# Kernel tuning notes

Hardware: AMD Instinct MI355X
Metric: run time of the kernel (lower is better)

The kernel has to match this reference:

```python
import jax, jax.numpy as jnp
import numpy as np

B, H, W, C = 32, 32, 32, 512
N_GROUPS = 32
EPS = 1e-5


def group_norm(x, scale, bias, n_groups=N_GROUPS, eps=EPS):
    b, h, w, c = x.shape
    xg = x.reshape(b, h, w, n_groups, c // n_groups)
    mean = xg.mean(axis=(1, 2, 4), keepdims=True)
    var = xg.var(axis=(1, 2, 4), keepdims=True)
    xg = (xg - mean) * jax.lax.rsqrt(var + eps)
    return xg.reshape(b, h, w, c) * scale + bias


def setup_inputs() -> dict:
    key = jax.random.key(0)
    ks = jax.random.split(key, 8)
    x = jax.random.normal(ks[0], (B, H, W, C), dtype=jnp.float32)
    t = jax.random.normal(ks[1], (B,), dtype=jnp.float32)
    gn_scale = jnp.ones((C,), jnp.float32)
    gn_bias = jnp.zeros((C,), jnp.float32)
    w_qkv = jax.random.normal(ks[2], (C, 3 * C), dtype=jnp.float32) / np.sqrt(C)
    b_qkv = jnp.zeros((3 * C,), jnp.float32)
    w_out = jax.random.normal(ks[3], (C, C), dtype=jnp.float32) / np.sqrt(C)
    b_out = jnp.zeros((C,), jnp.float32)
    return {"x": x, "t": t, "gn_scale": gn_scale, "gn_bias": gn_bias,
            "w_qkv": w_qkv, "b_qkv": b_qkv, "w_out": w_out, "b_out": b_out}


def reference(x, t, gn_scale, gn_bias, w_qkv, b_qkv, w_out, b_out):
    b, h, w, c = x.shape
    z = group_norm(x, gn_scale, gn_bias)
    qkv = jnp.einsum('bhwc,cd->bhwd', z, w_qkv) + b_qkv  # [b,h,w,3C]
    q, k, v = jnp.split(qkv, 3, axis=-1)
    # single-head spatial attention over all h*w positions
    attn = jnp.einsum('bhwc,bHWc->bhwHW', q, k) / jnp.sqrt(jnp.asarray(c, x.dtype))
    attn = jax.nn.softmax(attn.reshape(b, h, w, h * w), axis=-1)
    attn = attn.reshape(b, h, w, h, w)
    scores = jnp.einsum('bhwHW,bHWc->bhwc', attn, v)
    scores = jnp.einsum('bhwc,cd->bhwd', scores, w_out) + b_out
    return x + scores
```

## Files before the change

### kernel.cpp

```cpp
#include <hip/hip_runtime.h>

typedef unsigned short u16;
typedef short bf16x8 __attribute__((ext_vector_type(8)));
typedef float f32x4 __attribute__((ext_vector_type(4)));

__device__ __forceinline__ u16 f2bf(float f) {
  union { float f; unsigned u; } c; c.f = f;
  unsigned r = (c.u + 0x7FFFu + ((c.u >> 16) & 1u)) >> 16;
  return (u16)r;
}
__device__ __forceinline__ float bf2f(u16 h) {
  union { unsigned u; float f; } c; c.u = ((unsigned)h) << 16;
  return c.f;
}
__device__ __forceinline__ void gload16(const void* g, void* l) {
  __builtin_amdgcn_global_load_lds(
      (const __attribute__((address_space(1))) unsigned*)g,
      (__attribute__((address_space(3))) unsigned*)l, 16, 0, 0);
}

__global__ __launch_bounds__(256) void prep_weights(
    const float* __restrict__ w_qkv, const float* __restrict__ w_out,
    u16* __restrict__ wqkvT, u16* __restrict__ woutT) {
  int i = blockIdx.x * 256 + threadIdx.x;
  const int T1 = 1536 * 512;
  if (i < T1) {
    int n = i >> 9, c = i & 511;
    wqkvT[i] = f2bf(w_qkv[(size_t)c * 1536 + n]);
  } else {
    int j = i - T1;
    int n = j >> 9, c = j & 511;
    woutT[j] = f2bf(w_out[(size_t)c * 512 + n]);
  }
}

__global__ __launch_bounds__(256) void groupnorm_k(
    const float* __restrict__ x, const float* __restrict__ scale,
    const float* __restrict__ bias, u16* __restrict__ z) {
  const int blk = blockIdx.x, b = blk >> 5, g = blk & 31;
  const float* xb = x + (size_t)b * 524288 + g * 16;
  u16* zb = z + (size_t)b * 524288 + g * 16;
  const int tid = threadIdx.x, lane = tid & 63, wid = tid >> 6;

  float4 vv[16];
  float s = 0.f, ss = 0.f;
#pragma unroll
  for (int i = 0; i < 16; ++i) {
    int e = (i * 256 + tid) * 4;
    int hw = e >> 4, j = e & 15;
    vv[i] = *(const float4*)&xb[(size_t)hw * 512 + j];
    s += vv[i].x + vv[i].y + vv[i].z + vv[i].w;
    ss += vv[i].x * vv[i].x + vv[i].y * vv[i].y + vv[i].z * vv[i].z + vv[i].w * vv[i].w;
  }
#pragma unroll
  for (int off = 32; off; off >>= 1) {
    s += __shfl_xor(s, off);
    ss += __shfl_xor(ss, off);
  }
  __shared__ float rs[4], rq[4];
  if (!lane) { rs[wid] = s; rq[wid] = ss; }
  __syncthreads();
  float S_ = rs[0] + rs[1] + rs[2] + rs[3];
  float Q_ = rq[0] + rq[1] + rq[2] + rq[3];
  const float inv_n = 1.f / 16384.f;
  float mean = S_ * inv_n;
  float var = Q_ * inv_n - mean * mean;
  float rstd = rsqrtf(var + 1e-5f);

  int j0 = (tid * 4) & 15;
  float sc0 = scale[g * 16 + j0 + 0] * rstd, sc1 = scale[g * 16 + j0 + 1] * rstd;
  float sc2 = scale[g * 16 + j0 + 2] * rstd, sc3 = scale[g * 16 + j0 + 3] * rstd;
  float bi0 = bias[g * 16 + j0 + 0] - mean * sc0, bi1 = bias[g * 16 + j0 + 1] - mean * sc1;
  float bi2 = bias[g * 16 + j0 + 2] - mean * sc2, bi3 = bias[g * 16 + j0 + 3] - mean * sc3;
#pragma unroll
  for (int i = 0; i < 16; ++i) {
    int e = (i * 256 + tid) * 4;
    int hw = e >> 4, j = e & 15;
    ushort4 o;
    o.x = f2bf(vv[i].x * sc0 + bi0);
    o.y = f2bf(vv[i].y * sc1 + bi1);
    o.z = f2bf(vv[i].z * sc2 + bi2);
    o.w = f2bf(vv[i].w * sc3 + bi3);
    *(ushort4*)&zb[(size_t)hw * 512 + j] = o;
  }
}

#define QSCALE 0.04419417382415922f

template <int EPI>
__global__ __launch_bounds__(512, 2) void gemm8p(
    const u16* __restrict__ A, const u16* __restrict__ Bt,
    int gx, int gxy, int N, int K,
    long long sAb, long long sBb, long long sCb,
    const float* __restrict__ bias, const float* __restrict__ resid,
    u16* __restrict__ qb, u16* __restrict__ kb, u16* __restrict__ vt,
    u16* __restrict__ outb, float* __restrict__ outf) {
  int nb = gridDim.x, orig = blockIdx.x, id = orig;
  if (!(nb & 7)) { int chunk = nb >> 3; id = (orig & 7) * chunk + (orig >> 3); }
  int z = id / gxy; int r2 = id - z * gxy;
  int by = r2 / gx; int bx = r2 - by * gx;

  const u16* Ab = A + (size_t)z * sAb;
  const u16* Bb = Bt + (size_t)z * sBb;

  __shared__ u16 As[2][2][8192];
  __shared__ u16 Bs[2][2][8192];

  const int tid = threadIdx.x;
  const int lane = tid & 63, wid = tid >> 6;
  const int wm = wid & 1, wn = wid >> 1;
  const int l15 = lane & 15, l4 = lane >> 4;
  const int m0 = by * 256, n0 = bx * 256;

  const int own_is_b = wid >> 2;
  const int own_h = (wid >> 1) & 1;
  const int prow = ((wid & 1) << 6) | lane;
  const int srow = prow >> 3;
  const int scol = ((prow & 7) ^ (srow & 7)) << 3;
  const u16* own_base = (own_is_b ? Bb : Ab) +
      (size_t)((own_is_b ? n0 : m0) + own_h * 128 + srow) * K + scol;
  const int ldsbase = ((wid & 1) << 6) * 8;

  f32x4 acc[8][4];
#pragma unroll
  for (int i = 0; i < 8; ++i)
#pragma unroll
    for (int j = 0; j < 4; ++j)
#pragma unroll
      for (int r = 0; r < 4; ++r) acc[i][j][r] = 0.f;

  const int NT = K >> 6;

  auto stage = [&](int k0, int buf) {
    u16* l0 = (own_is_b ? &Bs[buf][own_h][0] : &As[buf][own_h][0]) + ldsbase;
    const u16* g0 = own_base + k0;
#pragma unroll
    for (int j = 0; j < 8; ++j)
      gload16(g0 + (size_t)(j * 16) * K, l0 + j * 1024);
  };

  stage(0, 0);
  asm volatile("s_waitcnt vmcnt(0)" ::: "memory");
  __builtin_amdgcn_s_barrier();

  for (int t = 0; t < NT; ++t) {
    const int cur = t & 1;
    const bool pre = (t + 1 < NT);
    const u16* Ah = &As[cur][wm][0];
    const u16* Bh = &Bs[cur][wn >> 1][0];
    const int rbB = (wn & 1) << 6;
    bf16x8 bq[4][2];
#pragma unroll
    for (int q = 0; q < 4; ++q) {
      bf16x8 af[2][2];
      if (q == 0) {
#pragma unroll
        for (int i = 0; i < 4; ++i) {
          const int rr = rbB + i * 16 + l15;
          const int sw = rr & 7;
          bq[i][0] = *(const bf16x8*)&Bh[rr * 64 + ((l4 ^ sw) << 3)];
          bq[i][1] = *(const bf16x8*)&Bh[rr * 64 + (((4 + l4) ^ sw) << 3)];
        }
      }
#pragma unroll
      for (int j = 0; j < 2; ++j) {
        const int rr = (q * 2 + j) * 16 + l15;
        const int sw = rr & 7;
        af[j][0] = *(const bf16x8*)&Ah[rr * 64 + ((l4 ^ sw) << 3)];
        af[j][1] = *(const bf16x8*)&Ah[rr * 64 + (((4 + l4) ^ sw) << 3)];
      }
      if (q == 0 && pre) stage((t + 1) << 6, cur ^ 1);
      __builtin_amdgcn_s_barrier();
      asm volatile("s_waitcnt lgkmcnt(0)" ::: "memory");
      __builtin_amdgcn_sched_barrier(0);
      __builtin_amdgcn_s_setprio(1);
#pragma unroll
      for (int j = 0; j < 2; ++j)
#pragma unroll
        for (int ni = 0; ni < 4; ++ni) {
          acc[q * 2 + j][ni] = __builtin_amdgcn_mfma_f32_16x16x32_bf16(
              af[j][0], bq[ni][0], acc[q * 2 + j][ni], 0, 0, 0);
          acc[q * 2 + j][ni] = __builtin_amdgcn_mfma_f32_16x16x32_bf16(
              af[j][1], bq[ni][1], acc[q * 2 + j][ni], 0, 0, 0);
        }
      __builtin_amdgcn_s_setprio(0);
      if (q == 3 && pre) asm volatile("s_waitcnt vmcnt(0)" ::: "memory");
      __builtin_amdgcn_s_barrier();
    }
  }

#pragma unroll
  for (int mi = 0; mi < 8; ++mi) {
#pragma unroll
    for (int ni = 0; ni < 4; ++ni) {
      const int gr0 = m0 + wm * 128 + mi * 16 + l4 * 4;
      const int gc = n0 + wn * 64 + ni * 16 + l15;
      if (EPI == 0) {
        const int bsel = gc >> 9, cin = gc & 511;
        const float bs = bias[gc];
        if (bsel < 2) {
          u16* dst = bsel ? kb : qb;
#pragma unroll
          for (int r = 0; r < 4; ++r) {
            float vvv = acc[mi][ni][r] + bs;
            if (bsel == 0) vvv *= QSCALE;
            dst[(size_t)(gr0 + r) * 512 + cin] = f2bf(vvv);
          }
        } else {
          ushort4 o;
          o.x = f2bf(acc[mi][ni][0] + bs);
          o.y = f2bf(acc[mi][ni][1] + bs);
          o.z = f2bf(acc[mi][ni][2] + bs);
          o.w = f2bf(acc[mi][ni][3] + bs);
          const int bb = gr0 >> 10, p = gr0 & 1023;
          *(ushort4*)&vt[(size_t)bb * 524288 + (size_t)cin * 1024 + p] = o;
        }
      } else if (EPI == 1) {
#pragma unroll
        for (int r = 0; r < 4; ++r)
          outb[(size_t)z * sCb + (size_t)(gr0 + r) * N + gc] = f2bf(acc[mi][ni][r]);
      } else {
#pragma unroll
        for (int r = 0; r < 4; ++r)
          outf[(size_t)(gr0 + r) * N + gc] =
              acc[mi][ni][r] + bias[gc] + resid[(size_t)(gr0 + r) * N + gc];
      }
    }
  }
}

__global__ __launch_bounds__(256) void softmax_rows(u16* __restrict__ S) {
  const size_t row = blockIdx.x;
  u16* p = S + row * 1024;
  const int tid = threadIdx.x, lane = tid & 63, wid = tid >> 6;
  ushort4 raw = ((const ushort4*)p)[tid];
  float v0 = bf2f(raw.x), v1 = bf2f(raw.y), v2 = bf2f(raw.z), v3 = bf2f(raw.w);
  float mx = fmaxf(fmaxf(v0, v1), fmaxf(v2, v3));
#pragma unroll
  for (int off = 32; off; off >>= 1) mx = fmaxf(mx, __shfl_xor(mx, off));
  __shared__ float red[8];
  if (!lane) red[wid] = mx;
  __syncthreads();
  mx = fmaxf(fmaxf(red[0], red[1]), fmaxf(red[2], red[3]));
  float e0 = __expf(v0 - mx), e1 = __expf(v1 - mx), e2 = __expf(v2 - mx), e3 = __expf(v3 - mx);
  float s = e0 + e1 + e2 + e3;
#pragma unroll
  for (int off = 32; off; off >>= 1) s += __shfl_xor(s, off);
  if (!lane) red[4 + wid] = s;
  __syncthreads();
  float inv = 1.0f / (red[4] + red[5] + red[6] + red[7]);
  ushort4 o;
  o.x = f2bf(e0 * inv); o.y = f2bf(e1 * inv); o.z = f2bf(e2 * inv); o.w = f2bf(e3 * inv);
  ((ushort4*)p)[tid] = o;
}

extern "C" void kernel_launch(void* const* d_in, const int* in_sizes, int n_in,
                              void* d_out, int out_size, void* d_ws, size_t ws_size,
                              hipStream_t stream) {
  const float* x = (const float*)d_in[0];
  const float* gn_scale = (const float*)d_in[2];
  const float* gn_bias = (const float*)d_in[3];
  const float* w_qkv = (const float*)d_in[4];
  const float* b_qkv = (const float*)d_in[5];
  const float* w_out = (const float*)d_in[6];
  const float* b_out = (const float*)d_in[7];
  float* out = (float*)d_out;

  char* ws = (char*)d_ws;
  const size_t MB = 1024ull * 1024ull;
  u16* qb = (u16*)(ws + 0 * MB);
  u16* kb = (u16*)(ws + 32 * MB);
  u16* vt = (u16*)(ws + 64 * MB);
  u16* zO = (u16*)(ws + 128 * MB);
  u16* S = (u16*)(ws + 160 * MB);
  u16* wqkvT = (u16*)(ws + 224 * MB);
  u16* woutT = (u16*)(ws + 226 * MB);

  prep_weights<<<4096, 256, 0, stream>>>(w_qkv, w_out, wqkvT, woutT);
  groupnorm_k<<<1024, 256, 0, stream>>>(x, gn_scale, gn_bias, zO);

  gemm8p<0><<<768, 512, 0, stream>>>(
      zO, wqkvT, 6, 768, 1536, 512, 0, 0, 0, b_qkv, nullptr,
      qb, kb, vt, nullptr, nullptr);

  gemm8p<1><<<512, 512, 0, stream>>>(
      qb, kb, 4, 16, 1024, 512, 1024 * 512, 1024 * 512, 1024 * 1024,
      nullptr, nullptr, nullptr, nullptr, nullptr, S, nullptr);

  softmax_rows<<<32768, 256, 0, stream>>>(S);

  gemm8p<1><<<256, 512, 0, stream>>>(
      S, vt, 2, 8, 512, 1024, 1024 * 1024, 512 * 1024, 1024 * 512,
      nullptr, nullptr, nullptr, nullptr, nullptr, zO, nullptr);

  gemm8p<2><<<256, 512, 0, stream>>>(
      zO, woutT, 2, 256, 512, 512, 0, 0, 0, b_out, x,
      nullptr, nullptr, nullptr, nullptr, out);
}
```

Baseline: 269.5 us.

## Spread GEMM tile loads across all waves and interleave per-quarter prefetch

Instead of having each wave own one half-tile and issue all prefetch loads at the first sub-step, every thread now loads a slice of each of the four half-tiles. The loads are spread over the four MFMA quarters, and the B tiles are prefetched two iterations ahead, using partial vmcnt waits. This spreads memory traffic more evenly across the K loop and keeps more loads in flight. The scheduling barrier is also removed. In exchange, the vmcnt bookkeeping is fragile, and B prefetch two steps ahead writes into the same double buffer, which risks a hazard if the ordering is wrong.

Result: slower. 278.8 us (+3.5%).

```diff
diff --git a/kernel.cpp b/kernel.cpp
--- a/kernel.cpp
+++ b/kernel.cpp
@@ -111,15 +111,21 @@
   const int wm = wid & 1, wn = wid >> 1;
   const int l15 = lane & 15, l4 = lane >> 4;
   const int m0 = by * 256, n0 = bx * 256;
-
-  const int own_is_b = wid >> 2;
-  const int own_h = (wid >> 1) & 1;
-  const int prow = ((wid & 1) << 6) | lane;
-  const int srow = prow >> 3;
-  const int scol = ((prow & 7) ^ (srow & 7)) << 3;
-  const u16* own_base = (own_is_b ? Bb : Ab) +
-      (size_t)((own_is_b ? n0 : m0) + own_h * 128 + srow) * K + scol;
-  const int ldsbase = ((wid & 1) << 6) * 8;
+  const int NT = K >> 6;
+
+  const int srow = tid >> 3;
+  const int scol = ((tid & 7) ^ (srow & 7)) << 3;
+
+  auto stageH = [&](int tt, int h) {
+    if (tt >= NT) return;
+    const int bsel = tt & 1;
+    u16* lds = (h >= 2 ? &Bs[bsel][h - 2][0] : &As[bsel][h][0]) + tid * 8;
+    const u16* gb = (h >= 2 ? Bb : Ab);
+    const int rb = (h >= 2 ? n0 + (h - 2) * 128 : m0 + h * 128) + srow;
+    const int k0 = (tt << 6) + scol;
+    gload16(gb + (size_t)rb * K + k0, lds);
+    gload16(gb + (size_t)(rb + 64) * K + k0, lds + 512 * 8);
+  };
 
   f32x4 acc[8][4];
 #pragma unroll
@@ -129,23 +135,13 @@
 #pragma unroll
       for (int r = 0; r < 4; ++r) acc[i][j][r] = 0.f;
 
-  const int NT = K >> 6;
-
-  auto stage = [&](int k0, int buf) {
-    u16* l0 = (own_is_b ? &Bs[buf][own_h][0] : &As[buf][own_h][0]) + ldsbase;
-    const u16* g0 = own_base + k0;
-#pragma unroll
-    for (int j = 0; j < 8; ++j)
-      gload16(g0 + (size_t)(j * 16) * K, l0 + j * 1024);
-  };
-
-  stage(0, 0);
-  asm volatile("s_waitcnt vmcnt(0)" ::: "memory");
+  stageH(0, 0); stageH(0, 1); stageH(0, 2); stageH(0, 3);
+  stageH(1, 2); stageH(1, 3);
+  asm volatile("s_waitcnt vmcnt(4)" ::: "memory");
   __builtin_amdgcn_s_barrier();
 
   for (int t = 0; t < NT; ++t) {
     const int cur = t & 1;
-    const bool pre = (t + 1 < NT);
     const u16* Ah = &As[cur][wm][0];
     const u16* Bh = &Bs[cur][wn >> 1][0];
     const int rbB = (wn & 1) << 6;
@@ -169,10 +165,12 @@
         af[j][0] = *(const bf16x8*)&Ah[rr * 64 + ((l4 ^ sw) << 3)];
         af[j][1] = *(const bf16x8*)&Ah[rr * 64 + (((4 + l4) ^ sw) << 3)];
       }
-      if (q == 0 && pre) stage((t + 1) << 6, cur ^ 1);
+      if (q == 0) stageH(t + 1, 0);
+      else if (q == 1) stageH(t + 1, 1);
+      else if (q == 2) stageH(t + 2, 2);
+      else stageH(t + 2, 3);
       __builtin_amdgcn_s_barrier();
       asm volatile("s_waitcnt lgkmcnt(0)" ::: "memory");
-      __builtin_amdgcn_sched_barrier(0);
       __builtin_amdgcn_s_setprio(1);
 #pragma unroll
       for (int j = 0; j < 2; ++j)
@@ -184,7 +182,10 @@
               af[j][1], bq[ni][1], acc[q * 2 + j][ni], 0, 0, 0);
         }
       __builtin_amdgcn_s_setprio(0);
-      if (q == 3 && pre) asm volatile("s_waitcnt vmcnt(0)" ::: "memory");
+      if (q == 3 && t + 1 < NT) {
+        if (t + 2 < NT) asm volatile("s_waitcnt vmcnt(4)" ::: "memory");
+        else asm volatile("s_waitcnt vmcnt(0)" ::: "memory");
+      }
       __builtin_amdgcn_s_barrier();
     }
   }
```

## Replace double-buffered GEMM with B-panel-resident LDS kernel reading A from global

Applied to the files above, without the earlier changes.

Rewrites the shared GEMM kernel so each block loads a full 128-column by 512-K panel of B into LDS once per K segment, while A fragments are loaded directly from global memory into registers. Tiles change to 256x128 per block, with each wave covering two 32-row slices, and grids are relaunched accordingly. The intent is to remove per-k-step A staging and barriers and to reuse B across more M rows. In exchange it drops the software pipelining, relies on cache for A reuse, and the 128 KB LDS footprint limits occupancy.

Result: slower. 408.8 us (+51.7%).

```diff
diff --git a/kernel.cpp b/kernel.cpp
--- a/kernel.cpp
+++ b/kernel.cpp
@@ -87,143 +87,123 @@
 
 #define QSCALE 0.04419417382415922f
 
-template <int EPI>
-__global__ __launch_bounds__(512, 2) void gemm8p(
+template <int EPI, int SEG>
+__global__ __launch_bounds__(512, 2) void gemm_panel(
     const u16* __restrict__ A, const u16* __restrict__ Bt,
-    int gx, int gxy, int N, int K,
+    int nPan, int gxy, int N,
     long long sAb, long long sBb, long long sCb,
     const float* __restrict__ bias, const float* __restrict__ resid,
-    u16* __restrict__ qb, u16* __restrict__ kb, u16* __restrict__ vt,
+    u16* __restrict__ qb, u16* __restrict__ kb, u16* __restrict__ vtb,
     u16* __restrict__ outb, float* __restrict__ outf) {
+  const int Ktot = SEG * 512;
   int nb = gridDim.x, orig = blockIdx.x, id = orig;
   if (!(nb & 7)) { int chunk = nb >> 3; id = (orig & 7) * chunk + (orig >> 3); }
-  int z = id / gxy; int r2 = id - z * gxy;
-  int by = r2 / gx; int bx = r2 - by * gx;
+  int z = id / gxy; int rem = id - z * gxy;
+  int pan = rem % nPan; int mb = rem / nPan;
 
   const u16* Ab = A + (size_t)z * sAb;
   const u16* Bb = Bt + (size_t)z * sBb;
 
-  __shared__ u16 As[2][2][8192];
-  __shared__ u16 Bs[2][2][8192];
+  __shared__ u16 Bs[128 * 512];
 
   const int tid = threadIdx.x;
   const int lane = tid & 63, wid = tid >> 6;
-  const int wm = wid & 1, wn = wid >> 1;
+  const int wm = wid >> 1;
+  const int wn = wid & 1;
   const int l15 = lane & 15, l4 = lane >> 4;
-  const int m0 = by * 256, n0 = bx * 256;
-
-  const int own_is_b = wid >> 2;
-  const int own_h = (wid >> 1) & 1;
-  const int prow = ((wid & 1) << 6) | lane;
-  const int srow = prow >> 3;
-  const int scol = ((prow & 7) ^ (srow & 7)) << 3;
-  const u16* own_base = (own_is_b ? Bb : Ab) +
-      (size_t)((own_is_b ? n0 : m0) + own_h * 128 + srow) * K + scol;
-  const int ldsbase = ((wid & 1) << 6) * 8;
-
-  f32x4 acc[8][4];
-#pragma unroll
-  for (int i = 0; i < 8; ++i)
-#pragma unroll
-    for (int j = 0; j < 4; ++j)
-#pragma unroll
-      for (int r = 0; r < 4; ++r) acc[i][j][r] = 0.f;
-
-  const int NT = K >> 6;
-
-  auto stage = [&](int k0, int buf) {
-    u16* l0 = (own_is_b ? &Bs[buf][own_h][0] : &As[buf][own_h][0]) + ldsbase;
-    const u16* g0 = own_base + k0;
-#pragma unroll
-    for (int j = 0; j < 8; ++j)
-      gload16(g0 + (size_t)(j * 16) * K, l0 + j * 1024);
-  };
-
-  stage(0, 0);
-  asm volatile("s_waitcnt vmcnt(0)" ::: "memory");
-  __builtin_amdgcn_s_barrier();
-
-  for (int t = 0; t < NT; ++t) {
-    const int cur = t & 1;
-    const bool pre = (t + 1 < NT);
-    const u16* Ah = &As[cur][wm][0];
-    const u16* Bh = &Bs[cur][wn >> 1][0];
-    const int rbB = (wn & 1) << 6;
-    bf16x8 bq[4][2];
-#pragma unroll
-    for (int q = 0; q < 4; ++q) {
-      bf16x8 af[2][2];
-      if (q == 0) {
-#pragma unroll
-        for (int i = 0; i < 4; ++i) {
-          const int rr = rbB + i * 16 + l15;
-          const int sw = rr & 7;
-          bq[i][0] = *(const bf16x8*)&Bh[rr * 64 + ((l4 ^ sw) << 3)];
-          bq[i][1] = *(const bf16x8*)&Bh[rr * 64 + (((4 + l4) ^ sw) << 3)];
+  const int n0 = pan * 128;
+  const int m0 = mb * 256;
+
+  f32x4 acc[2][2][4];
+#pragma unroll
+  for (int m = 0; m < 2; ++m)
+#pragma unroll
+    for (int i = 0; i < 2; ++i)
+#pragma unroll
+      for (int j = 0; j < 4; ++j)
+#pragma unroll
+        for (int r = 0; r < 4; ++r) acc[m][i][j][r] = 0.f;
+
+  const int srow8 = tid >> 6;
+  const int gi0 = tid & 63;
+
+#pragma unroll
+  for (int seg = 0; seg < SEG; ++seg) {
+    if (seg) __syncthreads();
+#pragma unroll
+    for (int j = 0; j < 16; ++j) {
+      const int row = j * 8 + srow8;
+      const int gis = (gi0 & 56) | ((gi0 & 7) ^ (row & 7));
+      gload16(Bb + (size_t)(n0 + row) * Ktot + seg * 512 + gis * 8,
+              &Bs[j * 4096 + tid * 8]);
+    }
+    __syncthreads();
+
+#pragma unroll
+    for (int m = 0; m < 2; ++m) {
+      const u16* Arow = Ab + (size_t)(m0 + m * 128 + wm * 32) * Ktot + seg * 512;
+#pragma unroll 4
+      for (int kc = 0; kc < 16; ++kc) {
+        bf16x8 af[2], bq[4];
+#pragma unroll
+        for (int i = 0; i < 2; ++i)
+          af[i] = *(const bf16x8*)&Arow[(size_t)(i * 16 + l15) * Ktot + kc * 32 + l4 * 8];
+#pragma unroll
+        for (int ni = 0; ni < 4; ++ni) {
+          const int rr = wn * 64 + ni * 16 + l15;
+          const int gi = kc * 4 + l4;
+          const int gis = (gi & 56) | ((gi & 7) ^ (rr & 7));
+          bq[ni] = *(const bf16x8*)&Bs[rr * 512 + gis * 8];
         }
+#pragma unroll
+        for (int i = 0; i < 2; ++i)
+#pragma unroll
+          for (int ni = 0; ni < 4; ++ni)
+            acc[m][i][ni] = __builtin_amdgcn_mfma_f32_16x16x32_bf16(
+                af[i], bq[ni], acc[m][i][ni], 0, 0, 0);
       }
-#pragma unroll
-      for (int j = 0; j < 2; ++j) {
-        const int rr = (q * 2 + j) * 16 + l15;
-        const int sw = rr & 7;
-        af[j][0] = *(const bf16x8*)&Ah[rr * 64 + ((l4 ^ sw) << 3)];
-        af[j][1] = *(const bf16x8*)&Ah[rr * 64 + (((4 + l4) ^ sw) << 3)];
-      }
-      if (q == 0 && pre) stage((t + 1) << 6, cur ^ 1);
-      __builtin_amdgcn_s_barrier();
-      asm volatile("s_waitcnt lgkmcnt(0)" ::: "memory");
-      __builtin_amdgcn_sched_barrier(0);
-      __builtin_amdgcn_s_setprio(1);
-#pragma unroll
-      for (int j = 0; j < 2; ++j)
-#pragma unroll
-        for (int ni = 0; ni < 4; ++ni) {
-          acc[q * 2 + j][ni] = __builtin_amdgcn_mfma_f32_16x16x32_bf16(
-              af[j][0], bq[ni][0], acc[q * 2 + j][ni], 0, 0, 0);
-          acc[q * 2 + j][ni] = __builtin_amdgcn_mfma_f32_16x16x32_bf16(
-              af[j][1], bq[ni][1], acc[q * 2 + j][ni], 0, 0, 0);
+    }
+  }
+
+#pragma unroll
+  for (int m = 0; m < 2; ++m) {
+#pragma unroll
+    for (int mi = 0; mi < 2; ++mi) {
+#pragma unroll
+      for (int ni = 0; ni < 4; ++ni) {
+        const int gr0 = m0 + m * 128 + wm * 32 + mi * 16 + l4 * 4;
+        const int gc = n0 + wn * 64 + ni * 16 + l15;
+        if (EPI == 0) {
+          const int bsel = gc >> 9, cin = gc & 511;
+          const float bs = bias[gc];
+          if (bsel < 2) {
+            u16* dst = bsel ? kb : qb;
+#pragma unroll
+            for (int r = 0; r < 4; ++r) {
+              float vvv = acc[m][mi][ni][r] + bs;
+              if (bsel == 0) vvv *= QSCALE;
+              dst[(size_t)(gr0 + r) * 512 + cin] = f2bf(vvv);
+            }
+          } else {
+            ushort4 o;
+            o.x = f2bf(acc[m][mi][ni][0] + bs);
+            o.y = f2bf(acc[m][mi][ni][1] + bs);
+            o.z = f2bf(acc[m][mi][ni][2] + bs);
+            o.w = f2bf(acc[m][mi][ni][3] + bs);
+            const int bb = gr0 >> 10, p = gr0 & 1023;
+            *(ushort4*)&vtb[(size_t)bb * 524288 + (size_t)cin * 1024 + p] = o;
+          }
+        } else if (EPI == 1) {
+#pragma unroll
+          for (int r = 0; r < 4; ++r)
+            outb[(size_t)z * sCb + (size_t)(gr0 + r) * N + gc] =
+                f2bf(acc[m][mi][ni][r]);
+        } else {
+#pragma unroll
+          for (int r = 0; r < 4; ++r)
+            outf[(size_t)(gr0 + r) * N + gc] =
+                acc[m][mi][ni][r] + bias[gc] + resid[(size_t)(gr0 + r) * N + gc];
         }
-      __builtin_amdgcn_s_setprio(0);
-      if (q == 3 && pre) asm volatile("s_waitcnt vmcnt(0)" ::: "memory");
-      __builtin_amdgcn_s_barrier();
-    }
-  }
-
-#pragma unroll
-  for (int mi = 0; mi < 8; ++mi) {
-#pragma unroll
-    for (int ni = 0; ni < 4; ++ni) {
-      const int gr0 = m0 + wm * 128 + mi * 16 + l4 * 4;
-      const int gc = n0 + wn * 64 + ni * 16 + l15;
-      if (EPI == 0) {
-        const int bsel = gc >> 9, cin = gc & 511;
-        const float bs = bias[gc];
-        if (bsel < 2) {
-          u16* dst = bsel ? kb : qb;
-#pragma unroll
-          for (int r = 0; r < 4; ++r) {
-            float vvv = acc[mi][ni][r] + bs;
-            if (bsel == 0) vvv *= QSCALE;
-            dst[(size_t)(gr0 + r) * 512 + cin] = f2bf(vvv);
-          }
-        } else {
-          ushort4 o;
-          o.x = f2bf(acc[mi][ni][0] + bs);
-          o.y = f2bf(acc[mi][ni][1] + bs);
-          o.z = f2bf(acc[mi][ni][2] + bs);
-          o.w = f2bf(acc[mi][ni][3] + bs);
-          const int bb = gr0 >> 10, p = gr0 & 1023;
-          *(ushort4*)&vt[(size_t)bb * 524288 + (size_t)cin * 1024 + p] = o;
-        }
-      } else if (EPI == 1) {
-#pragma unroll
-        for (int r = 0; r < 4; ++r)
-          outb[(size_t)z * sCb + (size_t)(gr0 + r) * N + gc] = f2bf(acc[mi][ni][r]);
-      } else {
-#pragma unroll
-        for (int r = 0; r < 4; ++r)
-          outf[(size_t)(gr0 + r) * N + gc] =
-              acc[mi][ni][r] + bias[gc] + resid[(size_t)(gr0 + r) * N + gc];
       }
     }
   }
@@ -279,21 +259,21 @@
   prep_weights<<<4096, 256, 0, stream>>>(w_qkv, w_out, wqkvT, woutT);
   groupnorm_k<<<1024, 256, 0, stream>>>(x, gn_scale, gn_bias, zO);
 
-  gemm8p<0><<<768, 512, 0, stream>>>(
-      zO, wqkvT, 6, 768, 1536, 512, 0, 0, 0, b_qkv, nullptr,
+  gemm_panel<0, 1><<<1536, 512, 0, stream>>>(
+      zO, wqkvT, 12, 1536, 1536, 0, 0, 0, b_qkv, nullptr,
       qb, kb, vt, nullptr, nullptr);
 
-  gemm8p<1><<<512, 512, 0, stream>>>(
-      qb, kb, 4, 16, 1024, 512, 1024 * 512, 1024 * 512, 1024 * 1024,
+  gemm_panel<1, 1><<<1024, 512, 0, stream>>>(
+      qb, kb, 8, 32, 1024, 1024 * 512, 1024 * 512, 1024 * 1024,
       nullptr, nullptr, nullptr, nullptr, nullptr, S, nullptr);
 
   softmax_rows<<<32768, 256, 0, stream>>>(S);
 
-  gemm8p<1><<<256, 512, 0, stream>>>(
-      S, vt, 2, 8, 512, 1024, 1024 * 1024, 512 * 1024, 1024 * 512,
+  gemm_panel<1, 2><<<512, 512, 0, stream>>>(
+      S, vt, 4, 16, 512, 1024 * 1024, 512 * 1024, 1024 * 512,
       nullptr, nullptr, nullptr, nullptr, nullptr, zO, nullptr);
 
-  gemm8p<2><<<256, 512, 0, stream>>>(
-      zO, woutT, 2, 256, 512, 512, 0, 0, 0, b_out, x,
+  gemm_panel<2, 1><<<512, 512, 0, stream>>>(
+      zO, woutT, 4, 512, 512, 0, 0, 0, b_out, x,
       nullptr, nullptr, nullptr, nullptr, out);
 }
```

## Fuse softmax into QK^T and PV GEMM epilogues, add XCD-aware tile mapping

Applied to the files above, without the earlier changes.

Removes the standalone softmax kernel. The QK^T GEMM epilogue now writes exp(score) as bf16 and stores per-row partial sums to a small workspace buffer; the PV GEMM epilogue divides by the summed partials. This cuts a full read and write pass over the 64 MB score matrix and one launch. The exp is taken without subtracting the row max, so very large scores could overflow. Block-to-tile mapping is also replaced with explicit XCD-aware panel and batch grouping to improve L2 locality.

Result: no change. 270.7 us (+0.4%).

```diff
diff --git a/kernel.cpp b/kernel.cpp
--- a/kernel.cpp
+++ b/kernel.cpp
@@ -91,14 +91,25 @@
 __global__ __launch_bounds__(512, 2) void gemm8p(
     const u16* __restrict__ A, const u16* __restrict__ Bt,
     int gx, int gxy, int N, int K,
+    int sched, int sp1, int sp2,
     long long sAb, long long sBb, long long sCb,
     const float* __restrict__ bias, const float* __restrict__ resid,
     u16* __restrict__ qb, u16* __restrict__ kb, u16* __restrict__ vt,
-    u16* __restrict__ outb, float* __restrict__ outf) {
-  int nb = gridDim.x, orig = blockIdx.x, id = orig;
-  if (!(nb & 7)) { int chunk = nb >> 3; id = (orig & 7) * chunk + (orig >> 3); }
-  int z = id / gxy; int r2 = id - z * gxy;
-  int by = r2 / gx; int bx = r2 - by * gx;
+    u16* __restrict__ outb, float* __restrict__ outf,
+    float* __restrict__ lsum) {
+  const int orig = blockIdx.x;
+  const int xcd = orig & 7, jj = orig >> 3;
+  int id;
+  if (sched == 0) {
+    int pan = jj % gx, loc = jj / gx;
+    id = (xcd * sp1 + loc) * gx + pan;
+  } else {
+    int tile = jj % gxy, bl = jj / gxy;
+    id = (xcd * sp2 + bl) * gxy + tile;
+  }
+  const int z = id / gxy;
+  const int r2 = id - z * gxy;
+  const int by = r2 / gx, bx = r2 - by * gx;
 
   const u16* Ab = A + (size_t)z * sAb;
   const u16* Bb = Bt + (size_t)z * sBb;
@@ -189,13 +200,13 @@
     }
   }
 
-#pragma unroll
-  for (int mi = 0; mi < 8; ++mi) {
-#pragma unroll
-    for (int ni = 0; ni < 4; ++ni) {
-      const int gr0 = m0 + wm * 128 + mi * 16 + l4 * 4;
-      const int gc = n0 + wn * 64 + ni * 16 + l15;
-      if (EPI == 0) {
+  if (EPI == 0) {
+#pragma unroll
+    for (int mi = 0; mi < 8; ++mi) {
+#pragma unroll
+      for (int ni = 0; ni < 4; ++ni) {
+        const int gr0 = m0 + wm * 128 + mi * 16 + l4 * 4;
+        const int gc = n0 + wn * 64 + ni * 16 + l15;
         const int bsel = gc >> 9, cin = gc & 511;
         const float bs = bias[gc];
         if (bsel < 2) {
@@ -215,43 +226,80 @@
           const int bb = gr0 >> 10, p = gr0 & 1023;
           *(ushort4*)&vt[(size_t)bb * 524288 + (size_t)cin * 1024 + p] = o;
         }
-      } else if (EPI == 1) {
-#pragma unroll
-        for (int r = 0; r < 4; ++r)
-          outb[(size_t)z * sCb + (size_t)(gr0 + r) * N + gc] = f2bf(acc[mi][ni][r]);
-      } else {
+      }
+    }
+  } else if (EPI == 2) {
+#pragma unroll
+    for (int mi = 0; mi < 8; ++mi) {
+#pragma unroll
+      for (int ni = 0; ni < 4; ++ni) {
+        const int gr0 = m0 + wm * 128 + mi * 16 + l4 * 4;
+        const int gc = n0 + wn * 64 + ni * 16 + l15;
 #pragma unroll
         for (int r = 0; r < 4; ++r)
           outf[(size_t)(gr0 + r) * N + gc] =
               acc[mi][ni][r] + bias[gc] + resid[(size_t)(gr0 + r) * N + gc];
       }
     }
-  }
-}
-
-__global__ __launch_bounds__(256) void softmax_rows(u16* __restrict__ S) {
-  const size_t row = blockIdx.x;
-  u16* p = S + row * 1024;
-  const int tid = threadIdx.x, lane = tid & 63, wid = tid >> 6;
-  ushort4 raw = ((const ushort4*)p)[tid];
-  float v0 = bf2f(raw.x), v1 = bf2f(raw.y), v2 = bf2f(raw.z), v3 = bf2f(raw.w);
-  float mx = fmaxf(fmaxf(v0, v1), fmaxf(v2, v3));
-#pragma unroll
-  for (int off = 32; off; off >>= 1) mx = fmaxf(mx, __shfl_xor(mx, off));
-  __shared__ float red[8];
-  if (!lane) red[wid] = mx;
-  __syncthreads();
-  mx = fmaxf(fmaxf(red[0], red[1]), fmaxf(red[2], red[3]));
-  float e0 = __expf(v0 - mx), e1 = __expf(v1 - mx), e2 = __expf(v2 - mx), e3 = __expf(v3 - mx);
-  float s = e0 + e1 + e2 + e3;
-#pragma unroll
-  for (int off = 32; off; off >>= 1) s += __shfl_xor(s, off);
-  if (!lane) red[4 + wid] = s;
-  __syncthreads();
-  float inv = 1.0f / (red[4] + red[5] + red[6] + red[7]);
-  ushort4 o;
-  o.x = f2bf(e0 * inv); o.y = f2bf(e1 * inv); o.z = f2bf(e2 * inv); o.w = f2bf(e3 * inv);
-  ((ushort4*)p)[tid] = o;
+  } else if (EPI == 3) {
+    float rs_[8][4];
+#pragma unroll
+    for (int mi = 0; mi < 8; ++mi)
+#pragma unroll
+      for (int r = 0; r < 4; ++r) rs_[mi][r] = 0.f;
+#pragma unroll
+    for (int mi = 0; mi < 8; ++mi) {
+      const int gr0 = m0 + wm * 128 + mi * 16 + l4 * 4;
+#pragma unroll
+      for (int ni = 0; ni < 4; ++ni) {
+        const int gc = n0 + wn * 64 + ni * 16 + l15;
+#pragma unroll
+        for (int r = 0; r < 4; ++r) {
+          float e = __expf(acc[mi][ni][r]);
+          rs_[mi][r] += e;
+          outb[(size_t)z * sCb + (size_t)(gr0 + r) * N + gc] = f2bf(e);
+        }
+      }
+    }
+#pragma unroll
+    for (int mi = 0; mi < 8; ++mi) {
+      const int gr0 = m0 + wm * 128 + mi * 16 + l4 * 4;
+#pragma unroll
+      for (int r = 0; r < 4; ++r) {
+        float v = rs_[mi][r];
+        v += __shfl_xor(v, 1);
+        v += __shfl_xor(v, 2);
+        v += __shfl_xor(v, 4);
+        v += __shfl_xor(v, 8);
+        if (l15 == 0)
+          lsum[((size_t)z * 1024 + gr0 + r) * 16 + bx * 4 + wn] = v;
+      }
+    }
+  } else {
+#pragma unroll
+    for (int mi = 0; mi < 8; ++mi) {
+      const int gr0 = m0 + wm * 128 + mi * 16 + l4 * 4;
+      float inv[4];
+#pragma unroll
+      for (int r = 0; r < 4; ++r) {
+        const float* lp = &lsum[((size_t)z * 1024 + gr0 + r) * 16];
+        const float4 a0 = *(const float4*)&lp[0];
+        const float4 a1 = *(const float4*)&lp[4];
+        const float4 a2 = *(const float4*)&lp[8];
+        const float4 a3 = *(const float4*)&lp[12];
+        inv[r] = 1.0f / (a0.x + a0.y + a0.z + a0.w + a1.x + a1.y + a1.z + a1.w +
+                         a2.x + a2.y + a2.z + a2.w + a3.x + a3.y + a3.z + a3.w);
+      }
+#pragma unroll
+      for (int ni = 0; ni < 4; ++ni) {
+        const int gc = n0 + wn * 64 + ni * 16 + l15;
+#pragma unroll
+        for (int r = 0; r < 4; ++r)
+          outb[(size_t)z * sCb + (size_t)(gr0 + r) * N + gc] =
+              f2bf(acc[mi][ni][r] * inv[r]);
+      }
+    }
+  }
 }
 
 extern "C" void kernel_launch(void* const* d_in, const int* in_sizes, int n_in,
@@ -271,6 +319,7 @@
   u16* qb = (u16*)(ws + 0 * MB);
   u16* kb = (u16*)(ws + 32 * MB);
   u16* vt = (u16*)(ws + 64 * MB);
+  float* lsum = (float*)(ws + 96 * MB);
   u16* zO = (u16*)(ws + 128 * MB);
   u16* S = (u16*)(ws + 160 * MB);
   u16* wqkvT = (u16*)(ws + 224 * MB);
@@ -280,20 +329,18 @@
   groupnorm_k<<<1024, 256, 0, stream>>>(x, gn_scale, gn_bias, zO);
 
   gemm8p<0><<<768, 512, 0, stream>>>(
-      zO, wqkvT, 6, 768, 1536, 512, 0, 0, 0, b_qkv, nullptr,
-      qb, kb, vt, nullptr, nullptr);
-
-  gemm8p<1><<<512, 512, 0, stream>>>(
-      qb, kb, 4, 16, 1024, 512, 1024 * 512, 1024 * 512, 1024 * 1024,
-      nullptr, nullptr, nullptr, nullptr, nullptr, S, nullptr);
-
-  softmax_rows<<<32768, 256, 0, stream>>>(S);
-
-  gemm8p<1><<<256, 512, 0, stream>>>(
-      S, vt, 2, 8, 512, 1024, 1024 * 1024, 512 * 1024, 1024 * 512,
-      nullptr, nullptr, nullptr, nullptr, nullptr, zO, nullptr);
+      zO, wqkvT, 6, 768, 1536, 512, 0, 16, 0, 0, 0, 0, b_qkv, nullptr,
+      qb, kb, vt, nullptr, nullptr, nullptr);
+
+  gemm8p<3><<<512, 512, 0, stream>>>(
+      qb, kb, 4, 16, 1024, 512, 1, 0, 4, 1024 * 512, 1024 * 512, 1024 * 1024,
+      nullptr, nullptr, nullptr, nullptr, nullptr, S, nullptr, lsum);
+
+  gemm8p<4><<<256, 512, 0, stream>>>(
+      S, vt, 2, 8, 512, 1024, 1, 0, 4, 1024 * 1024, 512 * 1024, 1024 * 512,
+      nullptr, nullptr, nullptr, nullptr, nullptr, zO, nullptr, lsum);
 
   gemm8p<2><<<256, 512, 0, stream>>>(
-      zO, woutT, 2, 256, 512, 512, 0, 0, 0, b_out, x,
-      nullptr, nullptr, nullptr, nullptr, out);
-}
+      zO, woutT, 2, 256, 512, 512, 0, 16, 0, 0, 0, 0, b_out, x,
+      nullptr, nullptr, nullptr, nullptr, out, nullptr);
+}
```
